# Performance work log

Hardware: AMD Instinct MI355X
Metric: run time of the kernel (lower is better)

## Reference

```python
import jax, jax.numpy as jnp
import numpy as np

THRESH_SCALE = 0.05

def ste_ternary(w):
    # forward: quantize to {-1,0,+1}; backward: straight-through (identity)
    thr = THRESH_SCALE * jnp.mean(jnp.abs(w))
    q = jnp.where(w > thr, 1.0, jnp.where(w < -thr, -1.0, 0.0)).astype(w.dtype)
    return w + jax.lax.stop_gradient(q - w)

def setup_inputs() -> dict:
    key = jax.random.key(0)
    kx, kw = jax.random.split(key)
    x = jax.random.normal(kx, (8192, 4096), dtype=jnp.float32)
    weight = jax.random.normal(kw, (4096, 4096), dtype=jnp.float32) * 0.1
    return {"x": x, "weight": weight}

def reference(x, weight):
    w_t = ste_ternary(weight)          # [out, in] in {-1,0,+1}
    return x @ w_t.T                    # [tokens, out]
```

## Files before the change

kernel.cpp:

```cpp
#include <hip/hip_runtime.h>
#include <hip/hip_bf16.h>
#include <stdint.h>


typedef __attribute__((ext_vector_type(4))) int i32x4;

#define BM 128
#define BN 128
#define BKB 64

#define M_ROWS 8192
#define ABS_BLOCKS 1024

__device__ inline void gld_lds16(const void* g, void* l) {
  __builtin_amdgcn_global_load_lds(
      (__attribute__((address_space(1))) void*)g,
      (__attribute__((address_space(3))) void*)l,
      16, 0, 0);
}

__device__ inline int pack4(int a, int b, int c, int d) {
  return (a & 255) | ((b & 255) << 8) | ((c & 255) << 16) | (d << 24);
}

__device__ inline int q8(float v, float inv) {
  int q = __float2int_rn(v * inv);
  return q > 127 ? 127 : (q < -127 ? -127 : q);
}

__global__ __launch_bounds__(256) void prep_kernel(
    const float4* __restrict__ x, signed char* __restrict__ xq,
    float* __restrict__ steps, const float4* __restrict__ w, int wn4,
    double* __restrict__ sum) {
  if (blockIdx.x < M_ROWS) {
    const int row = blockIdx.x;
    const float4* xr = x + (size_t)row * 1024;
    float4 v[4];
    float amax = 0.0f;
#pragma unroll
    for (int j = 0; j < 4; ++j) {
      v[j] = xr[threadIdx.x + 256 * j];
      amax = fmaxf(amax, fmaxf(fmaxf(fabsf(v[j].x), fabsf(v[j].y)),
                               fmaxf(fabsf(v[j].z), fabsf(v[j].w))));
    }
#pragma unroll
    for (int off = 32; off > 0; off >>= 1)
      amax = fmaxf(amax, __shfl_down(amax, off, 64));
    __shared__ float wmax[4];
    const int lane = threadIdx.x & 63, wave = threadIdx.x >> 6;
    if (lane == 0) wmax[wave] = amax;
    __syncthreads();
    const float m = fmaxf(fmaxf(wmax[0], wmax[1]), fmaxf(wmax[2], wmax[3]));
    const float inv = m > 0.0f ? 127.0f / m : 0.0f;
    if (threadIdx.x == 0) steps[row] = m > 0.0f ? m / 127.0f : 0.0f;
    int* out = (int*)(xq + (size_t)row * 4096);
#pragma unroll
    for (int j = 0; j < 4; ++j) {
      out[threadIdx.x + 256 * j] = pack4(q8(v[j].x, inv), q8(v[j].y, inv),
                                         q8(v[j].z, inv), q8(v[j].w, inv));
    }
  } else {
    double s = 0.0;
    const int stride = ABS_BLOCKS * 256;
    for (int i = (blockIdx.x - M_ROWS) * 256 + threadIdx.x; i < wn4;
         i += stride) {
      float4 v = w[i];
      s += (double)((fabsf(v.x) + fabsf(v.y)) + (fabsf(v.z) + fabsf(v.w)));
    }
#pragma unroll
    for (int off = 32; off > 0; off >>= 1) s += __shfl_down(s, off, 64);
    __shared__ double wsum[4];
    const int lane = threadIdx.x & 63, wave = threadIdx.x >> 6;
    if (lane == 0) wsum[wave] = s;
    __syncthreads();
    if (threadIdx.x == 0) atomicAdd(sum, wsum[0] + wsum[1] + wsum[2] + wsum[3]);
  }
}

__global__ __launch_bounds__(256) void quant_kernel(
    const float4* __restrict__ w, const double* __restrict__ sum,
    int* __restrict__ q, int n4, double inv_n) {
  const float thr = (float)(0.05 * (*sum) * inv_n);
  const int stride = gridDim.x * blockDim.x;
  for (int i = blockIdx.x * blockDim.x + threadIdx.x; i < n4; i += stride) {
    float4 v = w[i];
    int a = v.x > thr ? 1 : (v.x < -thr ? -1 : 0);
    int b = v.y > thr ? 1 : (v.y < -thr ? -1 : 0);
    int c = v.z > thr ? 1 : (v.z < -thr ? -1 : 0);
    int d = v.w > thr ? 1 : (v.w < -thr ? -1 : 0);
    q[i] = pack4(a, b, c, d);
  }
}

__global__ __launch_bounds__(256, 2) void gemm_i8(
    const signed char* __restrict__ A, const signed char* __restrict__ B,
    const float* __restrict__ steps, float* __restrict__ C, int M, int N,
    int K) {
  __shared__ unsigned char As[BM * BKB];
  __shared__ unsigned char Bs[BN * BKB];

  const int tid = threadIdx.x;
  const int lane = tid & 63;
  const int wave = tid >> 6;

  const int bm = blockIdx.y * BM;
  const int bn = blockIdx.x * BN;

  const int ca0 = wave * 2;
  const int ca1 = wave * 2 + 1;
  const int rl = lane >> 2;
  const int bo = (lane & 3) * 16;

  const signed char* a0 = A + (size_t)(bm + ca0 * 16 + rl) * K + bo;
  const signed char* a1 = A + (size_t)(bm + ca1 * 16 + rl) * K + bo;
  const signed char* b0 = B + (size_t)(bn + ca0 * 16 + rl) * K + bo;
  const signed char* b1 = B + (size_t)(bn + ca1 * 16 + rl) * K + bo;

  unsigned char* la0 = &As[ca0 * 1024];
  unsigned char* la1 = &As[ca1 * 1024];
  unsigned char* lb0 = &Bs[ca0 * 1024];
  unsigned char* lb1 = &Bs[ca1 * 1024];

  const int wm = (wave >> 1) * 64;
  const int wn = (wave & 1) * 64;

  const int fr = lane & 15;
  const int fk = (lane >> 4) * 16;

  i32x4 acc[4][4] = {};

  for (int k0 = 0; k0 < K; k0 += BKB) {
    gld_lds16(a0 + k0, la0);
    gld_lds16(a1 + k0, la1);
    gld_lds16(b0 + k0, lb0);
    gld_lds16(b1 + k0, lb1);
    __syncthreads();

    i32x4 af[4], bfr[4];
#pragma unroll
    for (int i = 0; i < 4; ++i) {
      af[i]  = *(const i32x4*)(&As[(wm + i * 16 + fr) * BKB + fk]);
      bfr[i] = *(const i32x4*)(&Bs[(wn + i * 16 + fr) * BKB + fk]);
    }
#pragma unroll
    for (int mi = 0; mi < 4; ++mi)
#pragma unroll
      for (int ni = 0; ni < 4; ++ni)
        acc[mi][ni] = __builtin_amdgcn_mfma_i32_16x16x64_i8(
            af[mi], bfr[ni], acc[mi][ni], 0, 0, 0);
    __syncthreads();
  }

  const int cn = lane & 15;
  const int cm = (lane >> 4) * 4;
  float st[4][4];
#pragma unroll
  for (int mi = 0; mi < 4; ++mi)
#pragma unroll
    for (int r = 0; r < 4; ++r)
      st[mi][r] = steps[bm + wm + mi * 16 + cm + r];
#pragma unroll
  for (int mi = 0; mi < 4; ++mi) {
#pragma unroll
    for (int ni = 0; ni < 4; ++ni) {
#pragma unroll
      for (int r = 0; r < 4; ++r) {
        int m = bm + wm + mi * 16 + cm + r;
        int n = bn + wn + ni * 16 + cn;
        C[(size_t)m * N + n] = (float)acc[mi][ni][r] * st[mi][r];
      }
    }
  }
}

extern "C" void kernel_launch(void* const* d_in, const int* in_sizes, int n_in,
                              void* d_out, int out_size, void* d_ws,
                              size_t ws_size, hipStream_t stream) {
  const float* x = (const float*)d_in[0];
  const float* w = (const float*)d_in[1];
  float* out = (float*)d_out;

  const int K = 4096;
  const int N = 4096;
  const int M = in_sizes[0] / K;
  const int NW = in_sizes[1];

  char* ws = (char*)d_ws;
  double* d_sum = (double*)ws;
  float* steps = (float*)(ws + 256);
  signed char* qb = (signed char*)(ws + 65536);
  signed char* xq = qb + (size_t)N * K;

  hipMemsetAsync(d_sum, 0, sizeof(double), stream);
  prep_kernel<<<M_ROWS + ABS_BLOCKS, 256, 0, stream>>>(
      (const float4*)x, xq, steps, (const float4*)w, NW / 4, d_sum);
  quant_kernel<<<2048, 256, 0, stream>>>((const float4*)w, d_sum, (int*)qb,
                                         NW / 4, 1.0 / NW);
  dim3 grid(N / BN, M / BM);
  gemm_i8<<<grid, 256, 0, stream>>>(xq, qb, steps, out, M, N, K);
}
```

Measured before the change: 419.8 us.

## Rewrite int8 GEMM as 256x256 double-buffered, swizzled, 8-wave pipelined kernel

Replaces the 128x128 single-buffered int8 GEMM with a 256x256 tile, 512-thread kernel using 128-byte K-steps. Global-to-LDS loads for the next tile go into a second LDS buffer and are interleaved across four phases of MFMA work, with explicit vmcnt waits, barriers and setprio around the MFMA bursts. LDS columns are XOR-swizzled to avoid bank conflicts. The aim is to hide load latency and raise arithmetic intensity, at the cost of 128KB of LDS per block, a heavier register footprint, and hand-tuned wait counts that are fragile.

```diff
diff --git a/kernel.cpp b/kernel.cpp
--- a/kernel.cpp
+++ b/kernel.cpp
@@ -5,9 +5,8 @@
 
 typedef __attribute__((ext_vector_type(4))) int i32x4;
 
-#define BM 128
-#define BN 128
-#define BKB 64
+#define KDIM 4096
+#define NDIM 4096
 
 #define M_ROWS 8192
 #define ABS_BLOCKS 1024
@@ -92,82 +91,135 @@
   }
 }
 
-__global__ __launch_bounds__(256, 2) void gemm_i8(
+#define MFMA_I8 __builtin_amdgcn_mfma_i32_16x16x64_i8
+
+__global__ __launch_bounds__(512, 2) void gemm_i8_8p(
     const signed char* __restrict__ A, const signed char* __restrict__ B,
-    const float* __restrict__ steps, float* __restrict__ C, int M, int N,
-    int K) {
-  __shared__ unsigned char As[BM * BKB];
-  __shared__ unsigned char Bs[BN * BKB];
+    const float* __restrict__ steps, float* __restrict__ C, int M) {
+  __shared__ unsigned char lds[131072];
 
   const int tid = threadIdx.x;
   const int lane = tid & 63;
-  const int wave = tid >> 6;
-
-  const int bm = blockIdx.y * BM;
-  const int bn = blockIdx.x * BN;
-
-  const int ca0 = wave * 2;
-  const int ca1 = wave * 2 + 1;
-  const int rl = lane >> 2;
-  const int bo = (lane & 3) * 16;
-
-  const signed char* a0 = A + (size_t)(bm + ca0 * 16 + rl) * K + bo;
-  const signed char* a1 = A + (size_t)(bm + ca1 * 16 + rl) * K + bo;
-  const signed char* b0 = B + (size_t)(bn + ca0 * 16 + rl) * K + bo;
-  const signed char* b1 = B + (size_t)(bn + ca1 * 16 + rl) * K + bo;
-
-  unsigned char* la0 = &As[ca0 * 1024];
-  unsigned char* la1 = &As[ca1 * 1024];
-  unsigned char* lb0 = &Bs[ca0 * 1024];
-  unsigned char* lb1 = &Bs[ca1 * 1024];
-
-  const int wm = (wave >> 1) * 64;
-  const int wn = (wave & 1) * 64;
+  const int w = tid >> 6;
+
+  const int bm = blockIdx.y * 256;
+  const int bn = blockIdx.x * 256;
+
+  const int rL = lane >> 3;
+  const int csw = (((lane & 7) ^ rL) << 4);
+  const signed char* aBase = A + (size_t)(bm + w * 8 + rL) * KDIM + csw;
+  const signed char* bBase = B + (size_t)(bn + w * 8 + rL) * KDIM + csw;
+  unsigned char* const ldsA = lds;
+  unsigned char* const ldsB = lds + 65536;
 
   const int fr = lane & 15;
   const int fk = (lane >> 4) * 16;
-
-  i32x4 acc[4][4] = {};
-
-  for (int k0 = 0; k0 < K; k0 += BKB) {
-    gld_lds16(a0 + k0, la0);
-    gld_lds16(a1 + k0, la1);
-    gld_lds16(b0 + k0, lb0);
-    gld_lds16(b1 + k0, lb1);
-    __syncthreads();
-
-    i32x4 af[4], bfr[4];
-#pragma unroll
-    for (int i = 0; i < 4; ++i) {
-      af[i]  = *(const i32x4*)(&As[(wm + i * 16 + fr) * BKB + fk]);
-      bfr[i] = *(const i32x4*)(&Bs[(wn + i * 16 + fr) * BKB + fk]);
-    }
-#pragma unroll
-    for (int mi = 0; mi < 4; ++mi)
-#pragma unroll
-      for (int ni = 0; ni < 4; ++ni)
-        acc[mi][ni] = __builtin_amdgcn_mfma_i32_16x16x64_i8(
-            af[mi], bfr[ni], acc[mi][ni], 0, 0, 0);
-    __syncthreads();
+  const int xr = (lane & 7) << 4;
+  const int cc0 = fk ^ xr;
+  const int cc1 = (64 + fk) ^ xr;
+  const int wm = (w >> 2) * 128;
+  const int wn = (w & 3) * 64;
+  const int aro = (wm + fr) * 128;
+  const int bro = (wn + fr) * 128;
+
+  i32x4 acc[8][4] = {};
+
+  gld_lds16(bBase, ldsB + w * 1024);
+  gld_lds16(bBase + (size_t)64 * KDIM, ldsB + 8192 + w * 1024);
+  gld_lds16(bBase + (size_t)128 * KDIM, ldsB + 16384 + w * 1024);
+  gld_lds16(bBase + (size_t)192 * KDIM, ldsB + 16384 + 8192 + w * 1024);
+  gld_lds16(aBase, ldsA + w * 1024);
+  gld_lds16(aBase + (size_t)128 * KDIM, ldsA + 16384 + w * 1024);
+  gld_lds16(aBase + (size_t)64 * KDIM, ldsA + 8192 + w * 1024);
+  gld_lds16(aBase + (size_t)192 * KDIM, ldsA + 16384 + 8192 + w * 1024);
+  asm volatile("s_waitcnt vmcnt(2)" ::: "memory");
+  __builtin_amdgcn_s_barrier();
+
+  for (int t = 0; t < 32; ++t) {
+    const int b = t & 1;
+    const bool st = (t < 31);
+    const unsigned char* Ab = ldsA + b * 32768;
+    const unsigned char* Bb = ldsB + b * 32768;
+    unsigned char* An = ldsA + (b ^ 1) * 32768;
+    unsigned char* Bn = ldsB + (b ^ 1) * 32768;
+    const signed char* aS = aBase + (size_t)(t + 1) * 128;
+    const signed char* bS = bBase + (size_t)(t + 1) * 128;
+
+    i32x4 bfr[4][2];
+
+#pragma unroll
+    for (int q = 0; q < 4; ++q) {
+      if (q == 0) {
+#pragma unroll
+        for (int ni = 0; ni < 4; ++ni) {
+          bfr[ni][0] = *(const i32x4*)(Bb + bro + ni * 2048 + cc0);
+          bfr[ni][1] = *(const i32x4*)(Bb + bro + ni * 2048 + cc1);
+        }
+      }
+      i32x4 a00 = *(const i32x4*)(Ab + aro + (2 * q) * 2048 + cc0);
+      i32x4 a01 = *(const i32x4*)(Ab + aro + (2 * q) * 2048 + cc1);
+      i32x4 a10 = *(const i32x4*)(Ab + aro + (2 * q + 1) * 2048 + cc0);
+      i32x4 a11 = *(const i32x4*)(Ab + aro + (2 * q + 1) * 2048 + cc1);
+
+      if (st) {
+        if (q == 0) {
+          gld_lds16(bS, Bn + w * 1024);
+          gld_lds16(bS + (size_t)64 * KDIM, Bn + 8192 + w * 1024);
+        } else if (q == 1) {
+          gld_lds16(bS + (size_t)128 * KDIM, Bn + 16384 + w * 1024);
+          gld_lds16(bS + (size_t)192 * KDIM, Bn + 16384 + 8192 + w * 1024);
+        } else if (q == 2) {
+          gld_lds16(aS, An + w * 1024);
+          gld_lds16(aS + (size_t)128 * KDIM, An + 16384 + w * 1024);
+        } else {
+          gld_lds16(aS + (size_t)64 * KDIM, An + 8192 + w * 1024);
+          gld_lds16(aS + (size_t)192 * KDIM, An + 16384 + 8192 + w * 1024);
+        }
+      }
+
+      __builtin_amdgcn_s_barrier();
+      asm volatile("s_waitcnt lgkmcnt(0)" ::: "memory");
+      __builtin_amdgcn_s_setprio(1);
+#pragma unroll
+      for (int ni = 0; ni < 4; ++ni) {
+        acc[2 * q][ni] = MFMA_I8(a00, bfr[ni][0], acc[2 * q][ni], 0, 0, 0);
+        acc[2 * q][ni] = MFMA_I8(a01, bfr[ni][1], acc[2 * q][ni], 0, 0, 0);
+        acc[2 * q + 1][ni] =
+            MFMA_I8(a10, bfr[ni][0], acc[2 * q + 1][ni], 0, 0, 0);
+        acc[2 * q + 1][ni] =
+            MFMA_I8(a11, bfr[ni][1], acc[2 * q + 1][ni], 0, 0, 0);
+      }
+      __builtin_amdgcn_s_setprio(0);
+
+      if (q == 1) {
+        if (st)
+          asm volatile("s_waitcnt vmcnt(4)" ::: "memory");
+        else
+          asm volatile("s_waitcnt vmcnt(0)" ::: "memory");
+      }
+      if (q == 3 && st)
+        asm volatile("s_waitcnt vmcnt(2)" ::: "memory");
+      __builtin_amdgcn_s_barrier();
+    }
   }
 
   const int cn = lane & 15;
   const int cm = (lane >> 4) * 4;
-  float st[4][4];
-#pragma unroll
-  for (int mi = 0; mi < 4; ++mi)
+  float stp[8][4];
+#pragma unroll
+  for (int mi = 0; mi < 8; ++mi)
 #pragma unroll
     for (int r = 0; r < 4; ++r)
-      st[mi][r] = steps[bm + wm + mi * 16 + cm + r];
-#pragma unroll
-  for (int mi = 0; mi < 4; ++mi) {
+      stp[mi][r] = steps[bm + wm + mi * 16 + cm + r];
+#pragma unroll
+  for (int mi = 0; mi < 8; ++mi) {
 #pragma unroll
     for (int ni = 0; ni < 4; ++ni) {
 #pragma unroll
       for (int r = 0; r < 4; ++r) {
-        int m = bm + wm + mi * 16 + cm + r;
-        int n = bn + wn + ni * 16 + cn;
-        C[(size_t)m * N + n] = (float)acc[mi][ni][r] * st[mi][r];
+        const int m = bm + wm + mi * 16 + cm + r;
+        const int n = bn + wn + ni * 16 + cn;
+        C[(size_t)m * NDIM + n] = (float)acc[mi][ni][r] * stp[mi][r];
       }
     }
   }
@@ -196,6 +248,6 @@
       (const float4*)x, xq, steps, (const float4*)w, NW / 4, d_sum);
   quant_kernel<<<2048, 256, 0, stream>>>((const float4*)w, d_sum, (int*)qb,
                                          NW / 4, 1.0 / NW);
-  dim3 grid(N / BN, M / BM);
-  gemm_i8<<<grid, 256, 0, stream>>>(xq, qb, steps, out, M, N, K);
-}
+  dim3 grid(N / 256, M / 256);
+  gemm_i8_8p<<<grid, 512, 0, stream>>>(xq, qb, steps, out, M);
+}
```

Result: faster. 389.2 us (-7.3%).
